# Kernel optimization log

Measured on AMD Instinct MI355X. Metric: run time of the kernel, lower is better.

Reference implementation:

```python
import jax, jax.numpy as jnp
import numpy as np

N = 100000      # nodes
E = 3200000     # edges (before self loops)
IN, H, OUT = 512, 256, 64
K = 10
TEMP = 1.5
EPS = 1e-5


def setup_inputs() -> dict:
    key = jax.random.key(0)
    ks = jax.random.split(key, 16)
    def lin(k, fan_in, fan_out):
        lim = 1.0 / np.sqrt(fan_in)
        kw, kb = jax.random.split(k)
        w = jax.random.uniform(kw, (fan_in, fan_out), jnp.float32, -lim, lim)
        b = jax.random.uniform(kb, (fan_out,), jnp.float32, -lim, lim)
        return w, b
    w1, b1 = lin(ks[0], IN, H)
    w2, b2 = lin(ks[1], H, H)
    w3, b3 = lin(ks[2], H, H)
    w4, b4 = lin(ks[3], H, OUT)
    return {
        "x": jax.random.normal(ks[4], (N, IN), jnp.float32),
        "edge_index": jax.random.randint(ks[5], (2, E), 0, N, jnp.int64),
        "w1": w1, "b1": b1, "g1": jnp.ones((H,), jnp.float32), "be1": jnp.zeros((H,), jnp.float32),
        "w2": w2, "b2": b2, "g2": jnp.ones((H,), jnp.float32), "be2": jnp.zeros((H,), jnp.float32),
        "w3": w3, "b3": b3, "g3": jnp.ones((H,), jnp.float32), "be3": jnp.zeros((H,), jnp.float32),
        "w4": w4, "b4": b4,
        "alpha": jnp.full((K + 1,), 1.0 / (K + 1), jnp.float32),
    }


def _bn(h, g, b):
    # batch-statistics BatchNorm1d (training-mode normalization, biased var)
    m = h.mean(axis=0)
    v = ((h - m) ** 2).mean(axis=0)
    return g * (h - m) * jax.lax.rsqrt(v + EPS) + b


def reference(x, edge_index, w1, b1, g1, be1, w2, b2, g2, be2,
              w3, b3, g3, be3, w4, b4, alpha):
    n = x.shape[0]
    # add self loops
    loop = jnp.arange(n, dtype=edge_index.dtype)
    row = jnp.concatenate([edge_index[0], loop])
    col = jnp.concatenate([edge_index[1], loop])
    # symmetric normalization D^{-1/2} A D^{-1/2} (degree counted on row)
    deg = jax.ops.segment_sum(jnp.ones_like(row, x.dtype), row, num_segments=n)
    dinv = jnp.where(deg > 0, jax.lax.rsqrt(deg), 0.0)
    norm = dinv[row] * dinv[col]  # [E+N]

    gelu = lambda h: jax.nn.gelu(h, approximate=False)
    x0 = gelu(_bn(x @ w1 + b1, g1, be1))
    x1 = gelu(_bn(x0 @ w2 + b2, g2, be2) + x0)   # dropout=identity (eval)
    x2 = gelu(_bn(x1 @ w3 + b3, g3, be3) + x1)
    h = x2 @ w4 + b4                              # [N, OUT]

    def step(carry, a):
        xt, acc = carry
        xt = jax.ops.segment_sum(norm[:, None] * xt[col], row, num_segments=n)
        return (xt, acc + a * xt), None

    (_, acc), _ = jax.lax.scan(step, (h, alpha[0] * h), alpha[1:])
    return acc / TEMP
```

## Files before the change

kernel.cpp:

```cpp
#include <hip/hip_runtime.h>
#include <math.h>

#define N_NODES 100000
#define N_IN 512
#define N_H 256
#define N_OUT 64
#define KHOP 10
#define EPS_BN 1e-5f
#define INV_TEMP (1.0f/1.5f)

using half8  = __attribute__((ext_vector_type(8))) _Float16;
using half4  = __attribute__((ext_vector_type(4))) _Float16;
using floatx4 = __attribute__((ext_vector_type(4))) float;

struct ZPtrs { const _Float16* p[KHOP]; };


__global__ void init_kernel(int* __restrict__ deg, int* __restrict__ cursor, int n) {
    int i = blockIdx.x * blockDim.x + threadIdx.x;
    if (i < n) { deg[i] = 1; cursor[i] = 0; }
}

__global__ void count_kernel(const int* __restrict__ ei, int* __restrict__ deg, int E) {
    int i = blockIdx.x * blockDim.x + threadIdx.x;
    if (i < E) atomicAdd(&deg[ei[i]], 1);
}

__global__ void scan1_kernel(const int* __restrict__ deg, int* __restrict__ excl,
                             int* __restrict__ bsum, int n) {
    __shared__ int sd[256];
    int t = threadIdx.x;
    int base = blockIdx.x * 1024 + t * 4;
    int v0 = (base + 0 < n) ? deg[base + 0] : 0;
    int v1 = (base + 1 < n) ? deg[base + 1] : 0;
    int v2 = (base + 2 < n) ? deg[base + 2] : 0;
    int v3 = (base + 3 < n) ? deg[base + 3] : 0;
    int tot = v0 + v1 + v2 + v3;
    sd[t] = tot;
    __syncthreads();
    for (int off = 1; off < 256; off <<= 1) {
        int x = (t >= off) ? sd[t - off] : 0;
        __syncthreads();
        sd[t] += x;
        __syncthreads();
    }
    int run = sd[t] - tot;
    if (t == 255) bsum[blockIdx.x] = sd[t];
    if (base + 0 < n) excl[base + 0] = run; run += v0;
    if (base + 1 < n) excl[base + 1] = run; run += v1;
    if (base + 2 < n) excl[base + 2] = run; run += v2;
    if (base + 3 < n) excl[base + 3] = run;
}

__global__ void scan2_kernel(int* __restrict__ bsum, int nb) {
    __shared__ int sd[128];
    int t = threadIdx.x;
    int v = (t < nb) ? bsum[t] : 0;
    sd[t] = v;
    __syncthreads();
    for (int off = 1; off < 128; off <<= 1) {
        int x = (t >= off) ? sd[t - off] : 0;
        __syncthreads();
        sd[t] += x;
        __syncthreads();
    }
    if (t < nb) bsum[t] = sd[t] - v;
}

__global__ void scan3_kernel(int* __restrict__ row_ptr, const int* __restrict__ bsum,
                             const int* __restrict__ deg, float* __restrict__ dinv,
                             float* __restrict__ dinv2, float* __restrict__ sqd,
                             int n, int total) {
    int i = blockIdx.x * blockDim.x + threadIdx.x;
    if (i < n) {
        row_ptr[i] += bsum[i >> 10];
        float d = (float)deg[i];
        dinv[i]  = rsqrtf(d);
        dinv2[i] = 1.0f / d;
        sqd[i]   = sqrtf(d);
    }
    if (i == 0) row_ptr[n] = total;
}

__global__ void fill_kernel(const int* __restrict__ ei, int* __restrict__ cursor,
                            const int* __restrict__ row_ptr,
                            int* __restrict__ colv, int E, int n) {
    int i = blockIdx.x * blockDim.x + threadIdx.x;
    if (i >= E + n) return;
    int r, c;
    if (i < E) { r = ei[i]; c = ei[E + i]; }
    else       { r = i - E; c = r; }
    int pos = row_ptr[r] + atomicAdd(&cursor[r], 1);
    colv[pos] = c;
}


__global__ void cvt_f16_kernel(const float* __restrict__ in, _Float16* __restrict__ out,
                               int total4) {
    int i = blockIdx.x * blockDim.x + threadIdx.x;
    if (i >= total4) return;
    float4 v = reinterpret_cast<const float4*>(in)[i];
    half4 h;
    h.x = (_Float16)v.x; h.y = (_Float16)v.y; h.z = (_Float16)v.z; h.w = (_Float16)v.w;
    reinterpret_cast<half4*>(out)[i] = h;
}

__global__ void cvt_wT_kernel(const float* __restrict__ w, _Float16* __restrict__ wT,
                              int K, int N) {
    int i = blockIdx.x * blockDim.x + threadIdx.x;
    if (i >= K * N) return;
    int k = i / N, n = i - k * N;
    wT[(size_t)n * K + k] = (_Float16)w[i];
}


template<int KDIM, int NDIM, int BN, bool STATS, bool WRITE_Z>
__global__ __launch_bounds__(256) void gemm_mfma_kernel(
    const _Float16* __restrict__ A, const _Float16* __restrict__ BT,
    const float* __restrict__ bias, float* __restrict__ C, int M,
    float* __restrict__ sums, const float* __restrict__ dinv,
    _Float16* __restrict__ z0) {
    constexpr int BM = 128;
    constexpr int LDK = 40;
    constexpr int WTN = BN / 32;
    __shared__ _Float16 As[BM * LDK];
    __shared__ _Float16 Bs[BN * LDK];
    __shared__ float cs[BN];
    __shared__ float cq[BN];
    int t = threadIdx.x;
    int mbase = blockIdx.y * BM;
    int nbase = blockIdx.x * BN;
    int wv = t >> 6, lane = t & 63;
    int wm = (wv & 1) * 64;
    int wn = (wv >> 1) * (BN / 2);
    int q = lane >> 4;
    int fr = lane & 15;
    int sr = t >> 2;
    int sc = (t & 3) * 8;

    floatx4 acc[4][WTN];
    for (int mt = 0; mt < 4; ++mt)
        for (int nt = 0; nt < WTN; ++nt)
            acc[mt][nt] = floatx4{0.f, 0.f, 0.f, 0.f};

    for (int k0 = 0; k0 < KDIM; k0 += 32) {
        #pragma unroll
        for (int p = 0; p < 2; ++p) {
            int row = sr + p * 64;
            int grow = mbase + row;
            half8 v = {};
            if (grow < M)
                v = *reinterpret_cast<const half8*>(&A[(size_t)grow * KDIM + k0 + sc]);
            *reinterpret_cast<half8*>(&As[row * LDK + sc]) = v;
        }
        #pragma unroll
        for (int p = 0; p < BN / 64; ++p) {
            int row = sr + p * 64;
            half8 v = *reinterpret_cast<const half8*>(&BT[(size_t)(nbase + row) * KDIM + k0 + sc]);
            *reinterpret_cast<half8*>(&Bs[row * LDK + sc]) = v;
        }
        __syncthreads();
        half8 af[4], bf[WTN];
        #pragma unroll
        for (int mt = 0; mt < 4; ++mt)
            af[mt] = *reinterpret_cast<const half8*>(&As[(wm + mt * 16 + fr) * LDK + q * 8]);
        #pragma unroll
        for (int nt = 0; nt < WTN; ++nt)
            bf[nt] = *reinterpret_cast<const half8*>(&Bs[(wn + nt * 16 + fr) * LDK + q * 8]);
        #pragma unroll
        for (int mt = 0; mt < 4; ++mt)
            #pragma unroll
            for (int nt = 0; nt < WTN; ++nt)
                acc[mt][nt] = __builtin_amdgcn_mfma_f32_16x16x32_f16(af[mt], bf[nt], acc[mt][nt], 0, 0, 0);
        __syncthreads();
    }
    if constexpr (STATS) {
        if (t < BN) { cs[t] = 0.f; cq[t] = 0.f; }
        __syncthreads();
    }
    #pragma unroll
    for (int nt = 0; nt < WTN; ++nt) {
        int col = nbase + wn + nt * 16 + fr;
        float bv = bias[col];
        float s = 0.f, s2 = 0.f;
        #pragma unroll
        for (int mt = 0; mt < 4; ++mt) {
            #pragma unroll
            for (int rr = 0; rr < 4; ++rr) {
                int row = mbase + wm + mt * 16 + q * 4 + rr;
                if (row < M) {
                    float v = acc[mt][nt][rr] + bv;
                    C[(size_t)row * NDIM + col] = v;
                    if constexpr (STATS) { s += v; s2 += v * v; }
                    if constexpr (WRITE_Z)
                        z0[((size_t)row << 6) + col] = (_Float16)(dinv[row] * v);
                }
            }
        }
        if constexpr (STATS) {
            s  += __shfl_xor(s, 16);  s  += __shfl_xor(s, 32);
            s2 += __shfl_xor(s2, 16); s2 += __shfl_xor(s2, 32);
            if (q == 0) {
                atomicAdd(&cs[wn + nt * 16 + fr], s);
                atomicAdd(&cq[wn + nt * 16 + fr], s2);
            }
        }
    }
    if constexpr (STATS) {
        __syncthreads();
        if (t < BN) {
            atomicAdd(&sums[nbase + t], cs[t]);
            atomicAdd(&sums[N_H + nbase + t], cq[t]);
        }
    }
}


__global__ void finalize_stats_kernel(const float* __restrict__ sums,
                                      const float* __restrict__ g, const float* __restrict__ be,
                                      float* __restrict__ ab, float invM) {
    int c = threadIdx.x;
    float mean = sums[c] * invM;
    float var = sums[N_H + c] * invM - mean * mean;
    float a = g[c] * rsqrtf(var + EPS_BN);
    ab[c] = a;
    ab[N_H + c] = be[c] - mean * a;
}

__global__ void bn_gelu_kernel(const float* __restrict__ T, const float* __restrict__ ab,
                               const _Float16* __restrict__ res, _Float16* __restrict__ Y,
                               int total4) {
    int i = blockIdx.x * blockDim.x + threadIdx.x;
    if (i >= total4) return;
    int c0 = (i * 4) & (N_H - 1);
    float4 tv = reinterpret_cast<const float4*>(T)[i];
    float4 av = *reinterpret_cast<const float4*>(&ab[c0]);
    float4 bv = *reinterpret_cast<const float4*>(&ab[N_H + c0]);
    float v0 = av.x * tv.x + bv.x;
    float v1 = av.y * tv.y + bv.y;
    float v2 = av.z * tv.z + bv.z;
    float v3 = av.w * tv.w + bv.w;
    if (res) {
        half4 rv = reinterpret_cast<const half4*>(res)[i];
        v0 += (float)rv.x; v1 += (float)rv.y; v2 += (float)rv.z; v3 += (float)rv.w;
    }
    half4 o;
    o.x = (_Float16)(0.5f * v0 * (1.f + erff(v0 * 0.70710678118654752f)));
    o.y = (_Float16)(0.5f * v1 * (1.f + erff(v1 * 0.70710678118654752f)));
    o.z = (_Float16)(0.5f * v2 * (1.f + erff(v2 * 0.70710678118654752f)));
    o.w = (_Float16)(0.5f * v3 * (1.f + erff(v3 * 0.70710678118654752f)));
    reinterpret_cast<half4*>(Y)[i] = o;
}


__global__ __launch_bounds__(256) void prop_kernel(
    const _Float16* __restrict__ zin, _Float16* __restrict__ zout,
    const int* __restrict__ colv, const int* __restrict__ row_ptr,
    const float* __restrict__ dinv2, int n) {
    int r = (blockIdx.x << 2) + (threadIdx.x >> 6);
    if (r >= n) return;
    int lane = threadIdx.x & 63;
    int s = __builtin_amdgcn_readfirstlane(row_ptr[r]);
    int e = __builtin_amdgcn_readfirstlane(row_ptr[r + 1]);
    float sum = 0.f;
    int i = s;
    for (; i + 8 <= e; i += 8) {
        int c0 = colv[i + 0], c1 = colv[i + 1], c2 = colv[i + 2], c3 = colv[i + 3];
        int c4 = colv[i + 4], c5 = colv[i + 5], c6 = colv[i + 6], c7 = colv[i + 7];
        float x0 = (float)zin[((size_t)c0 << 6) + lane];
        float x1 = (float)zin[((size_t)c1 << 6) + lane];
        float x2 = (float)zin[((size_t)c2 << 6) + lane];
        float x3 = (float)zin[((size_t)c3 << 6) + lane];
        float x4 = (float)zin[((size_t)c4 << 6) + lane];
        float x5 = (float)zin[((size_t)c5 << 6) + lane];
        float x6 = (float)zin[((size_t)c6 << 6) + lane];
        float x7 = (float)zin[((size_t)c7 << 6) + lane];
        sum += ((x0 + x1) + (x2 + x3)) + ((x4 + x5) + (x6 + x7));
    }
    for (; i < e; ++i)
        sum += (float)zin[((size_t)colv[i] << 6) + lane];
    float res = dinv2[r] * sum;
    zout[((size_t)r << 6) + lane] = (_Float16)res;
}

__global__ void prop_final_kernel(const float* __restrict__ h, ZPtrs zp,
                                  const float* __restrict__ sqd,
                                  const float* __restrict__ alpha,
                                  float* __restrict__ out, int total4) {
    int i = blockIdx.x * blockDim.x + threadIdx.x;
    if (i >= total4) return;
    int r = i >> 4;
    float4 hv = reinterpret_cast<const float4*>(h)[i];
    float s0 = 0.f, s1 = 0.f, s2 = 0.f, s3 = 0.f;
    #pragma unroll
    for (int k = 0; k < KHOP; ++k) {
        half4 z = reinterpret_cast<const half4*>(zp.p[k])[i];
        float ak = alpha[k + 1];
        s0 += ak * (float)z.x; s1 += ak * (float)z.y;
        s2 += ak * (float)z.z; s3 += ak * (float)z.w;
    }
    float sq = sqd[r];
    float a0 = alpha[0];
    float4 o;
    o.x = INV_TEMP * (a0 * hv.x + sq * s0);
    o.y = INV_TEMP * (a0 * hv.y + sq * s1);
    o.z = INV_TEMP * (a0 * hv.z + sq * s2);
    o.w = INV_TEMP * (a0 * hv.w + sq * s3);
    reinterpret_cast<float4*>(out)[i] = o;
}


extern "C" void kernel_launch(void* const* d_in, const int* in_sizes, int n_in,
                              void* d_out, int out_size, void* d_ws, size_t ws_size,
                              hipStream_t stream) {
    const float* x    = (const float*)d_in[0];
    const int*   ei   = (const int*)d_in[1];
    const float* w1   = (const float*)d_in[2];
    const float* b1   = (const float*)d_in[3];
    const float* g1   = (const float*)d_in[4];
    const float* be1  = (const float*)d_in[5];
    const float* w2   = (const float*)d_in[6];
    const float* b2   = (const float*)d_in[7];
    const float* g2   = (const float*)d_in[8];
    const float* be2  = (const float*)d_in[9];
    const float* w3   = (const float*)d_in[10];
    const float* b3   = (const float*)d_in[11];
    const float* g3   = (const float*)d_in[12];
    const float* be3  = (const float*)d_in[13];
    const float* w4   = (const float*)d_in[14];
    const float* b4   = (const float*)d_in[15];
    const float* alpha= (const float*)d_in[16];
    float* out = (float*)d_out;

    const int N = in_sizes[0] / N_IN;
    const int E = in_sizes[1] / 2;
    const int EN = E + N;
    const size_t NZ = (size_t)N * N_OUT;

    char* ws = (char*)d_ws;
    size_t off = 0;
    auto alloc = [&](size_t bytes) -> void* {
        void* p = ws + off;
        off = (off + bytes + 255) & ~(size_t)255;
        return p;
    };
    int*   deg     = (int*)alloc((size_t)N * 4);
    int*   cursor  = (int*)alloc((size_t)N * 4);
    int*   row_ptr = (int*)alloc((size_t)(N + 1) * 4);
    float* dinv    = (float*)alloc((size_t)N * 4);
    float* dinv2   = (float*)alloc((size_t)N * 4);
    float* sqd     = (float*)alloc((size_t)N * 4);
    int*   colv    = (int*)alloc((size_t)EN * 4);
    int*   bsum    = (int*)alloc(128 * 4);
    float* sums    = (float*)alloc(2 * N_H * 4);
    float* ab      = (float*)alloc(2 * N_H * 4);
    _Float16* w1T  = (_Float16*)alloc((size_t)N_IN * N_H * 2);
    _Float16* w2T  = (_Float16*)alloc((size_t)N_H * N_H * 2);
    _Float16* w3T  = (_Float16*)alloc((size_t)N_H * N_H * 2);
    _Float16* w4T  = (_Float16*)alloc((size_t)N_H * N_OUT * 2);
    _Float16* xh   = (_Float16*)alloc((size_t)N * N_IN * 2);
    float* T       = (float*)alloc((size_t)N * N_H * 4);
    _Float16* Ah0  = (_Float16*)alloc((size_t)N * N_H * 2);
    _Float16* Ah1  = (_Float16*)alloc((size_t)N * N_H * 2);
    float* hbuf    = (float*)alloc((size_t)N * N_OUT * 4);
    _Float16* z0   = (_Float16*)alloc(NZ * 2);

    _Float16* zk[KHOP + 1];
    zk[0] = z0;
    for (int k = 1; k <= 8; ++k) zk[k] = (_Float16*)T + (size_t)(k - 1) * NZ;
    zk[9]  = (_Float16*)Ah1;
    zk[10] = (_Float16*)Ah1 + NZ;

    const int TB = 256;
    int nbN  = (N + TB - 1) / TB;
    int nbE  = (E + TB - 1) / TB;
    int nbEN = (EN + TB - 1) / TB;
    int nscan = (N + 1023) / 1024;

    init_kernel<<<nbN, TB, 0, stream>>>(deg, cursor, N);
    count_kernel<<<nbE, TB, 0, stream>>>(ei, deg, E);
    scan1_kernel<<<nscan, TB, 0, stream>>>(deg, row_ptr, bsum, N);
    scan2_kernel<<<1, 128, 0, stream>>>(bsum, nscan);
    scan3_kernel<<<nbN, TB, 0, stream>>>(row_ptr, bsum, deg, dinv, dinv2, sqd, N, EN);
    fill_kernel<<<nbEN, TB, 0, stream>>>(ei, cursor, row_ptr, colv, E, N);

    int x4 = N * N_IN / 4;
    cvt_f16_kernel<<<(x4 + TB - 1) / TB, TB, 0, stream>>>(x, xh, x4);
    cvt_wT_kernel<<<(N_IN * N_H + TB - 1) / TB, TB, 0, stream>>>(w1, w1T, N_IN, N_H);
    cvt_wT_kernel<<<(N_H * N_H + TB - 1) / TB, TB, 0, stream>>>(w2, w2T, N_H, N_H);
    cvt_wT_kernel<<<(N_H * N_H + TB - 1) / TB, TB, 0, stream>>>(w3, w3T, N_H, N_H);
    cvt_wT_kernel<<<(N_H * N_OUT + TB - 1) / TB, TB, 0, stream>>>(w4, w4T, N_H, N_OUT);

    int mt = (N + 127) / 128;
    int elemH4 = N * N_H / 4;
    int nbElemH4 = (elemH4 + TB - 1) / TB;

    hipMemsetAsync(sums, 0, 2 * N_H * 4, stream);
    gemm_mfma_kernel<N_IN, N_H, 128, true, false><<<dim3(N_H / 128, mt), TB, 0, stream>>>(
        xh, w1T, b1, T, N, sums, nullptr, nullptr);
    finalize_stats_kernel<<<1, N_H, 0, stream>>>(sums, g1, be1, ab, 1.0f / N);
    bn_gelu_kernel<<<nbElemH4, TB, 0, stream>>>(T, ab, nullptr, Ah0, elemH4);
    hipMemsetAsync(sums, 0, 2 * N_H * 4, stream);
    gemm_mfma_kernel<N_H, N_H, 128, true, false><<<dim3(N_H / 128, mt), TB, 0, stream>>>(
        Ah0, w2T, b2, T, N, sums, nullptr, nullptr);
    finalize_stats_kernel<<<1, N_H, 0, stream>>>(sums, g2, be2, ab, 1.0f / N);
    bn_gelu_kernel<<<nbElemH4, TB, 0, stream>>>(T, ab, Ah0, Ah1, elemH4);
    hipMemsetAsync(sums, 0, 2 * N_H * 4, stream);
    gemm_mfma_kernel<N_H, N_H, 128, true, false><<<dim3(N_H / 128, mt), TB, 0, stream>>>(
        Ah1, w3T, b3, T, N, sums, nullptr, nullptr);
    finalize_stats_kernel<<<1, N_H, 0, stream>>>(sums, g3, be3, ab, 1.0f / N);
    bn_gelu_kernel<<<nbElemH4, TB, 0, stream>>>(T, ab, Ah1, Ah0, elemH4);
    gemm_mfma_kernel<N_H, N_OUT, 64, false, true><<<dim3(1, mt), TB, 0, stream>>>(
        Ah0, w4T, b4, hbuf, N, nullptr, dinv, z0);

    int nbProp = (N + 3) / 4;
    for (int k = 1; k <= KHOP; ++k) {
        prop_kernel<<<nbProp, TB, 0, stream>>>(zk[k - 1], zk[k], colv, row_ptr, dinv2, N);
    }

    ZPtrs zp;
    for (int k = 0; k < KHOP; ++k) zp.p[k] = zk[k + 1];
    int total4 = N * N_OUT / 4;
    prop_final_kernel<<<(total4 + TB - 1) / TB, TB, 0, stream>>>(hbuf, zp, sqd, alpha, out, total4);
}
```

Measured before the change: 1.688 ms.

## Store GEMM intermediates in fp16, vectorize gather in prop, partition CSR fill

GEMM outputs for the three hidden layers are now written as fp16 instead of fp32, and bn_gelu reads fp16, which halves intermediate traffic at some precision cost. The propagation kernel now has each wave handle four edges at once, with each lane loading half4 vectors, and combines the partial sums with cross-lane shuffles. The CSR fill is split into four row-range passes, each rereading all edges, so that atomics and scattered writes fall in a narrower region per pass, at the cost of extra edge reads. The fp16 store also changes the stats path: the sums are still taken from the fp32 values while the normalization is applied to rounded values.

Measured after the change: 1.641 ms. 1.03x faster.

```diff
diff --git a/kernel.cpp b/kernel.cpp
--- a/kernel.cpp
+++ b/kernel.cpp
@@ -84,12 +84,13 @@
 
 __global__ void fill_kernel(const int* __restrict__ ei, int* __restrict__ cursor,
                             const int* __restrict__ row_ptr,
-                            int* __restrict__ colv, int E, int n) {
+                            int* __restrict__ colv, int E, int n, int r0, int r1) {
     int i = blockIdx.x * blockDim.x + threadIdx.x;
     if (i >= E + n) return;
     int r, c;
     if (i < E) { r = ei[i]; c = ei[E + i]; }
     else       { r = i - E; c = r; }
+    if (r < r0 || r >= r1) return;
     int pos = row_ptr[r] + atomicAdd(&cursor[r], 1);
     colv[pos] = c;
 }
@@ -114,10 +115,10 @@
 }
 
 
-template<int KDIM, int NDIM, int BN, bool STATS, bool WRITE_Z>
+template<int KDIM, int NDIM, int BN, bool STATS, bool WRITE_Z, typename CT>
 __global__ __launch_bounds__(256) void gemm_mfma_kernel(
     const _Float16* __restrict__ A, const _Float16* __restrict__ BT,
-    const float* __restrict__ bias, float* __restrict__ C, int M,
+    const float* __restrict__ bias, CT* __restrict__ C, int M,
     float* __restrict__ sums, const float* __restrict__ dinv,
     _Float16* __restrict__ z0) {
     constexpr int BM = 128;
@@ -190,7 +191,7 @@
                 int row = mbase + wm + mt * 16 + q * 4 + rr;
                 if (row < M) {
                     float v = acc[mt][nt][rr] + bv;
-                    C[(size_t)row * NDIM + col] = v;
+                    C[(size_t)row * NDIM + col] = (CT)v;
                     if constexpr (STATS) { s += v; s2 += v * v; }
                     if constexpr (WRITE_Z)
                         z0[((size_t)row << 6) + col] = (_Float16)(dinv[row] * v);
@@ -227,19 +228,19 @@
     ab[N_H + c] = be[c] - mean * a;
 }
 
-__global__ void bn_gelu_kernel(const float* __restrict__ T, const float* __restrict__ ab,
+__global__ void bn_gelu_kernel(const _Float16* __restrict__ T, const float* __restrict__ ab,
                                const _Float16* __restrict__ res, _Float16* __restrict__ Y,
                                int total4) {
     int i = blockIdx.x * blockDim.x + threadIdx.x;
     if (i >= total4) return;
     int c0 = (i * 4) & (N_H - 1);
-    float4 tv = reinterpret_cast<const float4*>(T)[i];
+    half4 tv = reinterpret_cast<const half4*>(T)[i];
     float4 av = *reinterpret_cast<const float4*>(&ab[c0]);
     float4 bv = *reinterpret_cast<const float4*>(&ab[N_H + c0]);
-    float v0 = av.x * tv.x + bv.x;
-    float v1 = av.y * tv.y + bv.y;
-    float v2 = av.z * tv.z + bv.z;
-    float v3 = av.w * tv.w + bv.w;
+    float v0 = av.x * (float)tv.x + bv.x;
+    float v1 = av.y * (float)tv.y + bv.y;
+    float v2 = av.z * (float)tv.z + bv.z;
+    float v3 = av.w * (float)tv.w + bv.w;
     if (res) {
         half4 rv = reinterpret_cast<const half4*>(res)[i];
         v0 += (float)rv.x; v1 += (float)rv.y; v2 += (float)rv.z; v3 += (float)rv.w;
@@ -260,27 +261,48 @@
     int r = (blockIdx.x << 2) + (threadIdx.x >> 6);
     if (r >= n) return;
     int lane = threadIdx.x & 63;
+    int esub = lane >> 4;
+    int fo = (lane & 15) << 2;
     int s = __builtin_amdgcn_readfirstlane(row_ptr[r]);
     int e = __builtin_amdgcn_readfirstlane(row_ptr[r + 1]);
-    float sum = 0.f;
+    float a0 = 0.f, a1 = 0.f, a2 = 0.f, a3 = 0.f;
     int i = s;
-    for (; i + 8 <= e; i += 8) {
-        int c0 = colv[i + 0], c1 = colv[i + 1], c2 = colv[i + 2], c3 = colv[i + 3];
-        int c4 = colv[i + 4], c5 = colv[i + 5], c6 = colv[i + 6], c7 = colv[i + 7];
-        float x0 = (float)zin[((size_t)c0 << 6) + lane];
-        float x1 = (float)zin[((size_t)c1 << 6) + lane];
-        float x2 = (float)zin[((size_t)c2 << 6) + lane];
-        float x3 = (float)zin[((size_t)c3 << 6) + lane];
-        float x4 = (float)zin[((size_t)c4 << 6) + lane];
-        float x5 = (float)zin[((size_t)c5 << 6) + lane];
-        float x6 = (float)zin[((size_t)c6 << 6) + lane];
-        float x7 = (float)zin[((size_t)c7 << 6) + lane];
-        sum += ((x0 + x1) + (x2 + x3)) + ((x4 + x5) + (x6 + x7));
-    }
-    for (; i < e; ++i)
-        sum += (float)zin[((size_t)colv[i] << 6) + lane];
-    float res = dinv2[r] * sum;
-    zout[((size_t)r << 6) + lane] = (_Float16)res;
+    for (; i + 16 <= e; i += 16) {
+        int c0 = colv[i + esub];
+        int c1 = colv[i + 4 + esub];
+        int c2 = colv[i + 8 + esub];
+        int c3 = colv[i + 12 + esub];
+        half4 v0 = *reinterpret_cast<const half4*>(&zin[((size_t)c0 << 6) + fo]);
+        half4 v1 = *reinterpret_cast<const half4*>(&zin[((size_t)c1 << 6) + fo]);
+        half4 v2 = *reinterpret_cast<const half4*>(&zin[((size_t)c2 << 6) + fo]);
+        half4 v3 = *reinterpret_cast<const half4*>(&zin[((size_t)c3 << 6) + fo]);
+        a0 += (float)v0.x + (float)v1.x + (float)v2.x + (float)v3.x;
+        a1 += (float)v0.y + (float)v1.y + (float)v2.y + (float)v3.y;
+        a2 += (float)v0.z + (float)v1.z + (float)v2.z + (float)v3.z;
+        a3 += (float)v0.w + (float)v1.w + (float)v2.w + (float)v3.w;
+    }
+    for (; i + 4 <= e; i += 4) {
+        int c = colv[i + esub];
+        half4 v = *reinterpret_cast<const half4*>(&zin[((size_t)c << 6) + fo]);
+        a0 += (float)v.x; a1 += (float)v.y; a2 += (float)v.z; a3 += (float)v.w;
+    }
+    int rem = e - i;
+    if (esub < rem) {
+        int c = colv[i + esub];
+        half4 v = *reinterpret_cast<const half4*>(&zin[((size_t)c << 6) + fo]);
+        a0 += (float)v.x; a1 += (float)v.y; a2 += (float)v.z; a3 += (float)v.w;
+    }
+    a0 += __shfl_xor(a0, 16); a1 += __shfl_xor(a1, 16);
+    a2 += __shfl_xor(a2, 16); a3 += __shfl_xor(a3, 16);
+    a0 += __shfl_xor(a0, 32); a1 += __shfl_xor(a1, 32);
+    a2 += __shfl_xor(a2, 32); a3 += __shfl_xor(a3, 32);
+    if (lane < 16) {
+        float d = dinv2[r];
+        half4 o;
+        o.x = (_Float16)(a0 * d); o.y = (_Float16)(a1 * d);
+        o.z = (_Float16)(a2 * d); o.w = (_Float16)(a3 * d);
+        *reinterpret_cast<half4*>(&zout[((size_t)r << 6) + fo]) = o;
+    }
 }
 
 __global__ void prop_final_kernel(const float* __restrict__ h, ZPtrs zp,
@@ -365,6 +387,8 @@
     float* hbuf    = (float*)alloc((size_t)N * N_OUT * 4);
     _Float16* z0   = (_Float16*)alloc(NZ * 2);
 
+    _Float16* Tf16 = (_Float16*)T;
+
     _Float16* zk[KHOP + 1];
     zk[0] = z0;
     for (int k = 1; k <= 8; ++k) zk[k] = (_Float16*)T + (size_t)(k - 1) * NZ;
@@ -382,7 +406,15 @@
     scan1_kernel<<<nscan, TB, 0, stream>>>(deg, row_ptr, bsum, N);
     scan2_kernel<<<1, 128, 0, stream>>>(bsum, nscan);
     scan3_kernel<<<nbN, TB, 0, stream>>>(row_ptr, bsum, deg, dinv, dinv2, sqd, N, EN);
-    fill_kernel<<<nbEN, TB, 0, stream>>>(ei, cursor, row_ptr, colv, E, N);
+    {
+        const int P = 4;
+        int step = (N + P - 1) / P;
+        for (int p = 0; p < P; ++p) {
+            int r0 = p * step;
+            int r1 = min(N, r0 + step);
+            fill_kernel<<<nbEN, TB, 0, stream>>>(ei, cursor, row_ptr, colv, E, N, r0, r1);
+        }
+    }
 
     int x4 = N * N_IN / 4;
     cvt_f16_kernel<<<(x4 + TB - 1) / TB, TB, 0, stream>>>(x, xh, x4);
@@ -396,21 +428,21 @@
     int nbElemH4 = (elemH4 + TB - 1) / TB;
 
     hipMemsetAsync(sums, 0, 2 * N_H * 4, stream);
-    gemm_mfma_kernel<N_IN, N_H, 128, true, false><<<dim3(N_H / 128, mt), TB, 0, stream>>>(
-        xh, w1T, b1, T, N, sums, nullptr, nullptr);
+    gemm_mfma_kernel<N_IN, N_H, 128, true, false, _Float16><<<dim3(N_H / 128, mt), TB, 0, stream>>>(
+        xh, w1T, b1, Tf16, N, sums, nullptr, nullptr);
     finalize_stats_kernel<<<1, N_H, 0, stream>>>(sums, g1, be1, ab, 1.0f / N);
-    bn_gelu_kernel<<<nbElemH4, TB, 0, stream>>>(T, ab, nullptr, Ah0, elemH4);
+    bn_gelu_kernel<<<nbElemH4, TB, 0, stream>>>(Tf16, ab, nullptr, Ah0, elemH4);
     hipMemsetAsync(sums, 0, 2 * N_H * 4, stream);
-    gemm_mfma_kernel<N_H, N_H, 128, true, false><<<dim3(N_H / 128, mt), TB, 0, stream>>>(
-        Ah0, w2T, b2, T, N, sums, nullptr, nullptr);
+    gemm_mfma_kernel<N_H, N_H, 128, true, false, _Float16><<<dim3(N_H / 128, mt), TB, 0, stream>>>(
+        Ah0, w2T, b2, Tf16, N, sums, nullptr, nullptr);
     finalize_stats_kernel<<<1, N_H, 0, stream>>>(sums, g2, be2, ab, 1.0f / N);
-    bn_gelu_kernel<<<nbElemH4, TB, 0, stream>>>(T, ab, Ah0, Ah1, elemH4);
+    bn_gelu_kernel<<<nbElemH4, TB, 0, stream>>>(Tf16, ab, Ah0, Ah1, elemH4);
     hipMemsetAsync(sums, 0, 2 * N_H * 4, stream);
-    gemm_mfma_kernel<N_H, N_H, 128, true, false><<<dim3(N_H / 128, mt), TB, 0, stream>>>(
-        Ah1, w3T, b3, T, N, sums, nullptr, nullptr);
+    gemm_mfma_kernel<N_H, N_H, 128, true, false, _Float16><<<dim3(N_H / 128, mt), TB, 0, stream>>>(
+        Ah1, w3T, b3, Tf16, N, sums, nullptr, nullptr);
     finalize_stats_kernel<<<1, N_H, 0, stream>>>(sums, g3, be3, ab, 1.0f / N);
-    bn_gelu_kernel<<<nbElemH4, TB, 0, stream>>>(T, ab, Ah1, Ah0, elemH4);
-    gemm_mfma_kernel<N_H, N_OUT, 64, false, true><<<dim3(1, mt), TB, 0, stream>>>(
+    bn_gelu_kernel<<<nbElemH4, TB, 0, stream>>>(Tf16, ab, Ah1, Ah0, elemH4);
+    gemm_mfma_kernel<N_H, N_OUT, 64, false, true, float><<<dim3(1, mt), TB, 0, stream>>>(
         Ah0, w4T, b4, hbuf, N, nullptr, dinv, z0);
 
     int nbProp = (N + 3) / 4;
```
